# Optimization experiments

Hardware: AMD Instinct MI355X
Metric: run time of the kernel (lower is better)

The kernel has to match this reference:

```python
import jax, jax.numpy as jnp
import numpy as np

N_NODES = 100000
N_EDGES = 3200000
IN_DIM, HID_DIM, OUT_DIM = 384, 128, 5


def gcn_conv(x, src, dst, W, b, num_nodes):
    # PyG GCNConv: add self-loops, symmetric normalization, linear, aggregate, bias
    h = x @ W  # [N, out]
    ones = jnp.ones(src.shape[0], dtype=h.dtype)
    deg = jax.ops.segment_sum(ones, dst, num_segments=num_nodes)  # includes self-loops
    dinv = jnp.where(deg > 0, jax.lax.rsqrt(deg), 0.0)
    norm = dinv[src] * dinv[dst]  # [E+N]
    msg = h[src] * norm[:, None]
    out = jax.ops.segment_sum(msg, dst, num_segments=num_nodes)
    return out + b


def setup_inputs() -> dict:
    key = jax.random.key(0)
    ks = jax.random.split(key, 8)
    x = jax.random.normal(ks[0], (N_NODES, IN_DIM), dtype=jnp.float32)
    edge_index = jax.random.randint(ks[1], (2, N_EDGES), 0, N_NODES, dtype=jnp.int64)
    # Glorot-ish init for GCN linear weights
    def glorot(k, fi, fo):
        s = jnp.sqrt(6.0 / (fi + fo))
        return jax.random.uniform(k, (fi, fo), jnp.float32, -s, s)
    W1 = glorot(ks[2], IN_DIM, HID_DIM)
    b1 = jnp.zeros((HID_DIM,), jnp.float32)
    W2 = glorot(ks[3], HID_DIM, HID_DIM)
    b2 = jnp.zeros((HID_DIM,), jnp.float32)
    W3 = glorot(ks[4], HID_DIM, OUT_DIM)
    b3 = jnp.zeros((OUT_DIM,), jnp.float32)
    return {"x": x, "edge_index": edge_index, "W1": W1, "b1": b1,
            "W2": W2, "b2": b2, "W3": W3, "b3": b3}


def reference(x, edge_index, W1, b1, W2, b2, W3, b3):
    num_nodes = x.shape[0]
    loops = jnp.arange(num_nodes, dtype=edge_index.dtype)
    src = jnp.concatenate([edge_index[0], loops])
    dst = jnp.concatenate([edge_index[1], loops])
    # layer 1: GCNConv + ReLU (dropout is identity at inference)
    h = jax.nn.relu(gcn_conv(x, src, dst, W1, b1, num_nodes))
    # layer 2
    h = jax.nn.relu(gcn_conv(h, src, dst, W2, b2, num_nodes))
    # final layer: logits, no activation
    return gcn_conv(h, src, dst, W3, b3, num_nodes)
```

## Files before the change

kernel.cpp:

```cpp
#include <hip/hip_runtime.h>
#include <hip/hip_fp16.h>

#define NN 100000
#define NE 3200000
#define SCAN_CHUNK 1024

#define BSH 8
#define BKT_NODES 256
#define NBKT ((NN + BKT_NODES - 1) / BKT_NODES)
#define BIN_BLOCKS 256
#define EPB ((NE + BIN_BLOCKS - 1) / BIN_BLOCKS)
#define GH (NBKT * BIN_BLOCKS)

typedef unsigned int uint;
typedef unsigned short ushort;
typedef __attribute__((ext_vector_type(8))) _Float16 half8;
typedef __attribute__((ext_vector_type(4))) float f32x4;

__device__ inline void gload16(const void* g, void* l) {
    __builtin_amdgcn_global_load_lds(
        (const __attribute__((address_space(1))) void*)g,
        (__attribute__((address_space(3))) void*)l, 16, 0, 0);
}

__device__ inline uint f2h_pair(float a, float b) {
    return (uint)__half_as_ushort(__float2half(a)) |
           ((uint)__half_as_ushort(__float2half(b)) << 16);
}
__device__ inline float h2f_lo(uint u) { return __half2float(__ushort_as_half((ushort)(u & 0xFFFFu))); }
__device__ inline float h2f_hi(uint u) { return __half2float(__ushort_as_half((ushort)(u >> 16))); }
__device__ inline void splitH(float x, ushort& h, ushort& l) {
    __half hh = __float2half(x);
    h = __half_as_ushort(hh);
    l = __half_as_ushort(__float2half(x - __half2float(hh)));
}

__global__ __launch_bounds__(256) void hist_bkt(const int* __restrict__ dst,
                                                int* __restrict__ ghist) {
    __shared__ int h[NBKT];
    int t = threadIdx.x;
    for (int i = t; i < NBKT; i += 256) h[i] = 0;
    __syncthreads();
    int beg = blockIdx.x * EPB;
    int end = beg + EPB; if (end > NE) end = NE;
    for (int e = beg + t; e < end; e += 256)
        atomicAdd(&h[dst[e] >> BSH], 1);
    __syncthreads();
    for (int i = t; i < NBKT; i += 256)
        ghist[i * BIN_BLOCKS + blockIdx.x] = h[i];
}

__global__ __launch_bounds__(256) void scan_p1(const int* __restrict__ cnt,
                                               int* __restrict__ bsum, int N) {
    int t = threadIdx.x;
    int base = blockIdx.x * SCAN_CHUNK + t * 4;
    int s = 0;
#pragma unroll
    for (int q = 0; q < 4; q++) {
        int i = base + q;
        if (i < N) s += cnt[i];
    }
    __shared__ int red[4];
#pragma unroll
    for (int off = 32; off; off >>= 1) s += __shfl_down(s, off, 64);
    if ((t & 63) == 0) red[t >> 6] = s;
    __syncthreads();
    if (t == 0) bsum[blockIdx.x] = red[0] + red[1] + red[2] + red[3];
}

__global__ void scan_p2(int* __restrict__ bsum, int nb) {
    __shared__ int s[128];
    int t = threadIdx.x;
    int v = (t < nb) ? bsum[t] : 0;
    s[t] = v;
    __syncthreads();
    for (int off = 1; off < 128; off <<= 1) {
        int x = s[t];
        int add = (t >= off) ? s[t - off] : 0;
        __syncthreads();
        s[t] = x + add;
        __syncthreads();
    }
    if (t < nb) bsum[t] = s[t] - v;
}

__global__ __launch_bounds__(256) void scan_p3_plain(int* __restrict__ data,
                                                     const int* __restrict__ bsum, int N) {
    __shared__ int ts[256];
    int t = threadIdx.x;
    int base = blockIdx.x * SCAN_CHUNK + t * 4;
    int c[4];
    int s = 0;
#pragma unroll
    for (int q = 0; q < 4; q++) {
        int i = base + q;
        c[q] = (i < N) ? data[i] : 0;
        s += c[q];
    }
    ts[t] = s;
    __syncthreads();
    for (int off = 1; off < 256; off <<= 1) {
        int x = ts[t];
        int add = (t >= off) ? ts[t - off] : 0;
        __syncthreads();
        ts[t] = x + add;
        __syncthreads();
    }
    int run = bsum[blockIdx.x] + ts[t] - s;
#pragma unroll
    for (int q = 0; q < 4; q++) {
        int i = base + q;
        if (i < N) { data[i] = run; run += c[q]; }
    }
}

__global__ __launch_bounds__(256) void scan_p3_deg(const int* __restrict__ cnt,
                                                   const int* __restrict__ bsum,
                                                   int* __restrict__ rowptr,
                                                   float* __restrict__ dinv, int N) {
    __shared__ int ts[256];
    int t = threadIdx.x;
    int base = blockIdx.x * SCAN_CHUNK + t * 4;
    int c[4];
    int s = 0;
#pragma unroll
    for (int q = 0; q < 4; q++) {
        int i = base + q;
        c[q] = (i < N) ? cnt[i] : 0;
        s += c[q];
    }
    ts[t] = s;
    __syncthreads();
    for (int off = 1; off < 256; off <<= 1) {
        int x = ts[t];
        int add = (t >= off) ? ts[t - off] : 0;
        __syncthreads();
        ts[t] = x + add;
        __syncthreads();
    }
    int run = bsum[blockIdx.x] + ts[t] - s;
#pragma unroll
    for (int q = 0; q < 4; q++) {
        int i = base + q;
        if (i < N) {
            rowptr[i] = run;
            dinv[i] = 1.0f / sqrtf((float)(c[q] + 1));
            run += c[q];
        }
    }
    if (base < N && N <= base + 4) rowptr[N] = run;
}

__global__ __launch_bounds__(256) void bin_edges(const int* __restrict__ src,
                                                 const int* __restrict__ dst,
                                                 const int* __restrict__ ghist,
                                                 uint* __restrict__ binned) {
    __shared__ int cur[NBKT];
    int t = threadIdx.x;
    for (int i = t; i < NBKT; i += 256) cur[i] = ghist[i * BIN_BLOCKS + blockIdx.x];
    __syncthreads();
    int beg = blockIdx.x * EPB;
    int end = beg + EPB; if (end > NE) end = NE;
    for (int e = beg + t; e < end; e += 256) {
        int d = dst[e];
        int b = d >> BSH;
        int p = atomicAdd(&cur[b], 1);
        binned[p] = ((uint)src[e] << BSH) | (uint)(d & (BKT_NODES - 1));
    }
}

__global__ __launch_bounds__(256) void bucket_count(const uint* __restrict__ binned,
                                                    const int* __restrict__ ghist,
                                                    int* __restrict__ cnt) {
    __shared__ int c[BKT_NODES];
    int t = threadIdx.x;
    int bkt = blockIdx.x;
    for (int i = t; i < BKT_NODES; i += 256) c[i] = 0;
    __syncthreads();
    int beg = ghist[bkt * BIN_BLOCKS];
    int end = (bkt == NBKT - 1) ? NE : ghist[(bkt + 1) * BIN_BLOCKS];
    for (int j = beg + t; j < end; j += 256)
        atomicAdd(&c[binned[j] & (BKT_NODES - 1)], 1);
    __syncthreads();
    int base = bkt * BKT_NODES;
    int nb = NN - base; if (nb > BKT_NODES) nb = BKT_NODES;
    for (int i = t; i < nb; i += 256) cnt[base + i] = c[i];
}

__global__ __launch_bounds__(256) void csr_fill(const uint* __restrict__ binned,
                                                const int* __restrict__ ghist,
                                                const int* __restrict__ rowptr,
                                                int* __restrict__ col) {
    __shared__ int fill[BKT_NODES];
    int t = threadIdx.x;
    int bkt = blockIdx.x;
    for (int i = t; i < BKT_NODES; i += 256) fill[i] = 0;
    __syncthreads();
    int beg = ghist[bkt * BIN_BLOCKS];
    int end = (bkt == NBKT - 1) ? NE : ghist[(bkt + 1) * BIN_BLOCKS];
    int base = bkt * BKT_NODES;
    for (int j = beg + t; j < end; j += 256) {
        uint r = binned[j];
        int dl = r & (BKT_NODES - 1);
        int p = rowptr[base + dl] + atomicAdd(&fill[dl], 1);
        col[p] = (int)(r >> BSH);
    }
}

template <int K>
__global__ __launch_bounds__(256) void wsplit(const float* __restrict__ W,
                                              ushort* __restrict__ Wth,
                                              ushort* __restrict__ Wtl) {
    __shared__ float tile[32][128];
    int t = threadIdx.x;
    int kb = blockIdx.x;
    {
        int k = t >> 3, cq = t & 7;
#pragma unroll
        for (int q = 0; q < 4; q++) {
            float4 v = *(const float4*)&W[(size_t)(kb * 32 + k) * 128 + cq * 16 + q * 4];
            *(float4*)&tile[k][cq * 16 + q * 4] = v;
        }
    }
    __syncthreads();
    {
        int c = t >> 1, g = t & 1;
        ushort hs[16], ls[16];
#pragma unroll
        for (int i = 0; i < 16; i++) splitH(tile[g * 16 + i][c], hs[i], ls[i]);
        uint h[8], lo[8];
#pragma unroll
        for (int i = 0; i < 8; i++) {
            h[i] = (uint)hs[2 * i] | ((uint)hs[2 * i + 1] << 16);
            lo[i] = (uint)ls[2 * i] | ((uint)ls[2 * i + 1] << 16);
        }
        size_t o = (size_t)c * K + kb * 32 + g * 16;
        *(uint4*)&Wth[o] = make_uint4(h[0], h[1], h[2], h[3]);
        *(uint4*)&Wth[o + 8] = make_uint4(h[4], h[5], h[6], h[7]);
        *(uint4*)&Wtl[o] = make_uint4(lo[0], lo[1], lo[2], lo[3]);
        *(uint4*)&Wtl[o + 8] = make_uint4(lo[4], lo[5], lo[6], lo[7]);
    }
}

template <int K>
__global__ __launch_bounds__(256) void mfma_gemm_f32(const float* __restrict__ X,
                                                     const ushort* __restrict__ Wth,
                                                     const ushort* __restrict__ Wtl,
                                                     const float* __restrict__ dinv,
                                                     uint* __restrict__ Y, int M) {
    __shared__ char smem[24 * 1024];
    char* aP = smem;
    char* bH = smem + 8192;
    char* bL = smem + 16384;
    int tid = threadIdx.x;
    int w = tid >> 6, l = tid & 63;
    int rowBase = blockIdx.x * 128;

    f32x4 acc[2][8];
#pragma unroll
    for (int mf = 0; mf < 2; mf++)
#pragma unroll
        for (int n = 0; n < 8; n++) acc[mf][n] = (f32x4){0.f, 0.f, 0.f, 0.f};

    int sRow = tid >> 1, sKp = tid & 1;
    int gRow = rowBase + sRow;
    bool rowOK = gRow < M;
    size_t aBase = (size_t)(rowOK ? gRow : 0) * K + sKp * 16;

    float4 a0, a1, a2, a3;
    a0 = a1 = a2 = a3 = make_float4(0.f, 0.f, 0.f, 0.f);
    if (rowOK) {
        a0 = *(const float4*)&X[aBase];
        a1 = *(const float4*)&X[aBase + 4];
        a2 = *(const float4*)&X[aBase + 8];
        a3 = *(const float4*)&X[aBase + 12];
    }

    int fc = l & 15, fkg = l >> 4;
    int aoff0 = fkg * 2048 + ((2 * w + 0) * 16 + fc) * 16;
    int aoff1 = fkg * 2048 + ((2 * w + 1) * 16 + fc) * 16;

    for (int kt = 0; kt < K; kt += 32) {
#pragma unroll
        for (int i = 0; i < 2; i++) {
            int cb = (i * 4 + w) * 64;
            int c = cb + l;
            int kg = c >> 7, colb = c & 127;
            size_t go = (size_t)colb * K + kt + kg * 8;
            gload16(&Wth[go], bH + cb * 16);
            gload16(&Wtl[go], bL + cb * 16);
        }
        {
            float v[16] = {a0.x, a0.y, a0.z, a0.w, a1.x, a1.y, a1.z, a1.w,
                           a2.x, a2.y, a2.z, a2.w, a3.x, a3.y, a3.z, a3.w};
            uint hh[8];
#pragma unroll
            for (int i = 0; i < 8; i++) hh[i] = f2h_pair(v[2 * i], v[2 * i + 1]);
            *(uint4*)(aP + (2 * sKp) * 2048 + sRow * 16) = make_uint4(hh[0], hh[1], hh[2], hh[3]);
            *(uint4*)(aP + (2 * sKp + 1) * 2048 + sRow * 16) = make_uint4(hh[4], hh[5], hh[6], hh[7]);
        }
        __syncthreads();

        if (kt + 32 < K && rowOK) {
            size_t nb = aBase + kt + 32;
            a0 = *(const float4*)&X[nb];
            a1 = *(const float4*)&X[nb + 4];
            a2 = *(const float4*)&X[nb + 8];
            a3 = *(const float4*)&X[nb + 12];
        }

        half8 av0 = *(const half8*)(aP + aoff0);
        half8 av1 = *(const half8*)(aP + aoff1);
#pragma unroll
        for (int n = 0; n < 8; n++) {
            int boff = fkg * 2048 + (16 * n + fc) * 16;
            half8 bh = *(const half8*)(bH + boff);
            half8 bl = *(const half8*)(bL + boff);
            acc[0][n] = __builtin_amdgcn_mfma_f32_16x16x32_f16(av0, bh, acc[0][n], 0, 0, 0);
            acc[0][n] = __builtin_amdgcn_mfma_f32_16x16x32_f16(av0, bl, acc[0][n], 0, 0, 0);
            acc[1][n] = __builtin_amdgcn_mfma_f32_16x16x32_f16(av1, bh, acc[1][n], 0, 0, 0);
            acc[1][n] = __builtin_amdgcn_mfma_f32_16x16x32_f16(av1, bl, acc[1][n], 0, 0, 0);
        }
        __syncthreads();
    }

#pragma unroll
    for (int mf = 0; mf < 2; mf++) {
        float dscale[4];
#pragma unroll
        for (int r = 0; r < 4; r++) {
            int row = rowBase + (2 * w + mf) * 16 + fkg * 4 + r;
            dscale[r] = (row < M) ? dinv[row] : 0.f;
        }
#pragma unroll
        for (int n = 0; n < 8; n++) {
#pragma unroll
            for (int r = 0; r < 4; r++) {
                float val = acc[mf][n][r] * dscale[r];
                float p = __shfl_xor(val, 1, 64);
                int row = rowBase + (2 * w + mf) * 16 + fkg * 4 + r;
                if (!(l & 1) && row < M)
                    Y[(size_t)row * 64 + 8 * n + (fc >> 1)] = f2h_pair(val, p);
            }
        }
    }
}

__global__ __launch_bounds__(256) void mfma_gemm_f16(const ushort* __restrict__ Xh,
                                                     const ushort* __restrict__ Wth,
                                                     const ushort* __restrict__ Wtl,
                                                     const float* __restrict__ dinv,
                                                     uint* __restrict__ Y, int M) {
    __shared__ char smem[24 * 1024];
    char* aP = smem;
    char* bH = smem + 8192;
    char* bL = smem + 16384;
    int tid = threadIdx.x;
    int w = tid >> 6, l = tid & 63;
    int rowBase = blockIdx.x * 128;

    f32x4 acc[2][8];
#pragma unroll
    for (int mf = 0; mf < 2; mf++)
#pragma unroll
        for (int n = 0; n < 8; n++) acc[mf][n] = (f32x4){0.f, 0.f, 0.f, 0.f};

    int fc = l & 15, fkg = l >> 4;
    int aoff0 = fkg * 2048 + ((2 * w + 0) * 16 + fc) * 16;
    int aoff1 = fkg * 2048 + ((2 * w + 1) * 16 + fc) * 16;

    for (int kt = 0; kt < 128; kt += 32) {
#pragma unroll
        for (int i = 0; i < 2; i++) {
            int cb = (i * 4 + w) * 64;
            int c = cb + l;
            int kg = c >> 7, idx = c & 127;
            gload16(&Xh[(size_t)(rowBase + idx) * 128 + kt + kg * 8], aP + cb * 16);
            gload16(&Wth[(size_t)idx * 128 + kt + kg * 8], bH + cb * 16);
            gload16(&Wtl[(size_t)idx * 128 + kt + kg * 8], bL + cb * 16);
        }
        __syncthreads();
        half8 av0 = *(const half8*)(aP + aoff0);
        half8 av1 = *(const half8*)(aP + aoff1);
#pragma unroll
        for (int n = 0; n < 8; n++) {
            int boff = fkg * 2048 + (16 * n + fc) * 16;
            half8 bh = *(const half8*)(bH + boff);
            half8 bl = *(const half8*)(bL + boff);
            acc[0][n] = __builtin_amdgcn_mfma_f32_16x16x32_f16(av0, bh, acc[0][n], 0, 0, 0);
            acc[0][n] = __builtin_amdgcn_mfma_f32_16x16x32_f16(av0, bl, acc[0][n], 0, 0, 0);
            acc[1][n] = __builtin_amdgcn_mfma_f32_16x16x32_f16(av1, bh, acc[1][n], 0, 0, 0);
            acc[1][n] = __builtin_amdgcn_mfma_f32_16x16x32_f16(av1, bl, acc[1][n], 0, 0, 0);
        }
        __syncthreads();
    }

#pragma unroll
    for (int mf = 0; mf < 2; mf++) {
        float dscale[4];
#pragma unroll
        for (int r = 0; r < 4; r++) {
            int row = rowBase + (2 * w + mf) * 16 + fkg * 4 + r;
            dscale[r] = (row < M) ? dinv[row] : 0.f;
        }
#pragma unroll
        for (int n = 0; n < 8; n++) {
#pragma unroll
            for (int r = 0; r < 4; r++) {
                float val = acc[mf][n][r] * dscale[r];
                float p = __shfl_xor(val, 1, 64);
                int row = rowBase + (2 * w + mf) * 16 + fkg * 4 + r;
                if (!(l & 1) && row < M)
                    Y[(size_t)row * 64 + 8 * n + (fc >> 1)] = f2h_pair(val, p);
            }
        }
    }
}

__global__ __launch_bounds__(256) void gemm_n5h(const uint4* __restrict__ Xh,
                                                const float* __restrict__ W,
                                                float* __restrict__ Y, int M) {
    __shared__ float wl[640];
    int t = threadIdx.x;
    for (int i = t; i < 640; i += 256) wl[i] = W[i];
    __syncthreads();
    int row = blockIdx.x * 256 + t;
    if (row >= M) return;
    float acc0 = 0.f, acc1 = 0.f, acc2 = 0.f, acc3 = 0.f, acc4 = 0.f;
#pragma unroll
    for (int kq = 0; kq < 16; kq++) {
        uint4 v = Xh[(size_t)row * 16 + kq];
        uint uu[4] = {v.x, v.y, v.z, v.w};
#pragma unroll
        for (int e = 0; e < 4; e++) {
            float x0 = h2f_lo(uu[e]);
            float x1 = h2f_hi(uu[e]);
            int k = kq * 8 + e * 2;
            acc0 = fmaf(x0, wl[k * 5 + 0], acc0); acc0 = fmaf(x1, wl[k * 5 + 5], acc0);
            acc1 = fmaf(x0, wl[k * 5 + 1], acc1); acc1 = fmaf(x1, wl[k * 5 + 6], acc1);
            acc2 = fmaf(x0, wl[k * 5 + 2], acc2); acc2 = fmaf(x1, wl[k * 5 + 7], acc2);
            acc3 = fmaf(x0, wl[k * 5 + 3], acc3); acc3 = fmaf(x1, wl[k * 5 + 8], acc3);
            acc4 = fmaf(x0, wl[k * 5 + 4], acc4); acc4 = fmaf(x1, wl[k * 5 + 9], acc4);
        }
    }
    Y[row * 5 + 0] = acc0;
    Y[row * 5 + 1] = acc1;
    Y[row * 5 + 2] = acc2;
    Y[row * 5 + 3] = acc3;
    Y[row * 5 + 4] = acc4;
}

__global__ void pack5(const float* __restrict__ Y, const float* __restrict__ dinv,
                      uint4* __restrict__ hc, int N) {
    int node = blockIdx.x * 256 + threadIdx.x;
    if (node >= N) return;
    float di = dinv[node];
    float v0 = Y[node * 5 + 0] * di;
    float v1 = Y[node * 5 + 1] * di;
    float v2 = Y[node * 5 + 2] * di;
    float v3 = Y[node * 5 + 3] * di;
    float v4 = Y[node * 5 + 4] * di;
    hc[node] = make_uint4(f2h_pair(v0, v1), f2h_pair(v2, v3), f2h_pair(v4, 0.f), 0u);
}

#define ACC8H(v)                              \
    a0 += h2f_lo(v.x); a1 += h2f_hi(v.x);     \
    a2 += h2f_lo(v.y); a3 += h2f_hi(v.y);     \
    a4 += h2f_lo(v.z); a5 += h2f_hi(v.z);     \
    a6 += h2f_lo(v.w); a7 += h2f_hi(v.w);

__global__ __launch_bounds__(256) void agg128_v3(const uint4* __restrict__ hb4,
                                                 const int* __restrict__ rowptr,
                                                 const int* __restrict__ col,
                                                 const float* __restrict__ dinv,
                                                 const float* __restrict__ bias,
                                                 uint4* __restrict__ out, int N, int do_relu) {
    int wave = threadIdx.x >> 6;
    int lane = threadIdx.x & 63;
    int node = blockIdx.x * 4 + wave;
    if (node >= N) return;
    int g = lane >> 4;
    int q = lane & 15;
    int beg = rowptr[node], end = rowptr[node + 1];
    float a0 = 0.f, a1 = 0.f, a2 = 0.f, a3 = 0.f, a4 = 0.f, a5 = 0.f, a6 = 0.f, a7 = 0.f;

    int j = beg;
    for (; j + 16 <= end; j += 16) {
        int s0 = col[j + g];
        int s1 = col[j + 4 + g];
        int s2 = col[j + 8 + g];
        int s3 = col[j + 12 + g];
        uint4 v0 = hb4[(size_t)s0 * 16 + q];
        uint4 v1 = hb4[(size_t)s1 * 16 + q];
        uint4 v2 = hb4[(size_t)s2 * 16 + q];
        uint4 v3 = hb4[(size_t)s3 * 16 + q];
        ACC8H(v0); ACC8H(v1); ACC8H(v2); ACC8H(v3);
    }
    if (j + 8 <= end) {
        int s0 = col[j + g];
        int s1 = col[j + 4 + g];
        uint4 v0 = hb4[(size_t)s0 * 16 + q];
        uint4 v1 = hb4[(size_t)s1 * 16 + q];
        ACC8H(v0); ACC8H(v1);
        j += 8;
    }
    if (j < end) {
        int jj0 = j + g, jj1 = j + 4 + g;
        bool p0 = jj0 < end, p1 = jj1 < end;
        int s0 = p0 ? col[jj0] : node;
        int s1 = p1 ? col[jj1] : node;
        uint4 v0 = hb4[(size_t)s0 * 16 + q];
        uint4 v1 = hb4[(size_t)s1 * 16 + q];
        if (!p0) v0 = make_uint4(0u, 0u, 0u, 0u);
        if (!p1) v1 = make_uint4(0u, 0u, 0u, 0u);
        ACC8H(v0); ACC8H(v1);
    }
#pragma unroll
    for (int off = 16; off <= 32; off <<= 1) {
        a0 += __shfl_xor(a0, off, 64);
        a1 += __shfl_xor(a1, off, 64);
        a2 += __shfl_xor(a2, off, 64);
        a3 += __shfl_xor(a3, off, 64);
        a4 += __shfl_xor(a4, off, 64);
        a5 += __shfl_xor(a5, off, 64);
        a6 += __shfl_xor(a6, off, 64);
        a7 += __shfl_xor(a7, off, 64);
    }
    if (g == 0) {
        uint4 vs = hb4[(size_t)node * 16 + q];
        ACC8H(vs);
        float di = dinv[node];
        const float4* bias4 = (const float4*)bias;
        float4 bb0 = bias4[q * 2], bb1 = bias4[q * 2 + 1];
        float o0 = a0 * di + bb0.x, o1 = a1 * di + bb0.y;
        float o2 = a2 * di + bb0.z, o3 = a3 * di + bb0.w;
        float o4 = a4 * di + bb1.x, o5 = a5 * di + bb1.y;
        float o6 = a6 * di + bb1.z, o7 = a7 * di + bb1.w;
        if (do_relu) {
            o0 = fmaxf(o0, 0.f); o1 = fmaxf(o1, 0.f);
            o2 = fmaxf(o2, 0.f); o3 = fmaxf(o3, 0.f);
            o4 = fmaxf(o4, 0.f); o5 = fmaxf(o5, 0.f);
            o6 = fmaxf(o6, 0.f); o7 = fmaxf(o7, 0.f);
        }
        out[(size_t)node * 16 + q] =
            make_uint4(f2h_pair(o0, o1), f2h_pair(o2, o3), f2h_pair(o4, o5), f2h_pair(o6, o7));
    }
}

__global__ void agg5_v2(const uint4* __restrict__ hc, const int* __restrict__ rowptr,
                        const int* __restrict__ col, const float* __restrict__ dinv,
                        const float* __restrict__ b3, float* __restrict__ out, int N) {
    int node = blockIdx.x * 256 + threadIdx.x;
    if (node >= N) return;
    float a0 = 0.f, a1 = 0.f, a2 = 0.f, a3 = 0.f, a4 = 0.f;
    int beg = rowptr[node], end = rowptr[node + 1];
#pragma unroll 2
    for (int j = beg; j < end; ++j) {
        uint4 v = hc[col[j]];
        a0 += h2f_lo(v.x); a1 += h2f_hi(v.x);
        a2 += h2f_lo(v.y); a3 += h2f_hi(v.y);
        a4 += h2f_lo(v.z);
    }
    uint4 vs = hc[node];
    a0 += h2f_lo(vs.x); a1 += h2f_hi(vs.x);
    a2 += h2f_lo(vs.y); a3 += h2f_hi(vs.y);
    a4 += h2f_lo(vs.z);
    float di = dinv[node];
    out[node * 5 + 0] = a0 * di + b3[0];
    out[node * 5 + 1] = a1 * di + b3[1];
    out[node * 5 + 2] = a2 * di + b3[2];
    out[node * 5 + 3] = a3 * di + b3[3];
    out[node * 5 + 4] = a4 * di + b3[4];
}

static inline size_t align512(size_t x) { return (x + 511) & ~(size_t)511; }

extern "C" void kernel_launch(void* const* d_in, const int* in_sizes, int n_in,
                              void* d_out, int out_size, void* d_ws, size_t ws_size,
                              hipStream_t stream) {
    const float* x  = (const float*)d_in[0];
    const int* ei   = (const int*)d_in[1];
    const float* W1 = (const float*)d_in[2];
    const float* b1 = (const float*)d_in[3];
    const float* W2 = (const float*)d_in[4];
    const float* b2 = (const float*)d_in[5];
    const float* W3 = (const float*)d_in[6];
    const float* b3 = (const float*)d_in[7];
    const int* src = ei;
    const int* dst = ei + NE;

    char* ws = (char*)d_ws;
    size_t off = 0;
    int* cnt = (int*)(ws + off);        off += align512((size_t)NN * 4);
    int* rowptr = (int*)(ws + off);     off += align512((size_t)(NN + 1) * 4);
    float* dinv = (float*)(ws + off);   off += align512((size_t)NN * 4);
    int* bsum = (int*)(ws + off);       off += align512((size_t)128 * 4);
    int* ghist = (int*)(ws + off);      off += align512((size_t)GH * 4);
    ushort* wt1h = (ushort*)(ws + off); off += align512((size_t)128 * 384 * 2);
    ushort* wt1l = (ushort*)(ws + off); off += align512((size_t)128 * 384 * 2);
    ushort* wt2h = (ushort*)(ws + off); off += align512((size_t)128 * 128 * 2);
    ushort* wt2l = (ushort*)(ws + off); off += align512((size_t)128 * 128 * 2);
    int* col = (int*)(ws + off);        off += align512((size_t)NE * 4);
    uint* hb = (uint*)(ws + off);       off += align512((size_t)NN * 64 * 4);
    char* bufF = (char*)(ws + off);     off += align512((size_t)NN * 128 * 4);
    float* bufC = (float*)(ws + off);   off += align512((size_t)NN * 5 * 4);
    uint4* hc = (uint4*)(ws + off);     off += align512((size_t)NN * 16);
    uint* binned = (uint*)bufF;
    (void)ws_size;

    wsplit<384><<<12, 256, 0, stream>>>(W1, wt1h, wt1l);
    wsplit<128><<<4, 256, 0, stream>>>(W2, wt2h, wt2l);

    hist_bkt<<<BIN_BLOCKS, 256, 0, stream>>>(dst, ghist);
    {
        int nb = (GH + SCAN_CHUNK - 1) / SCAN_CHUNK;
        scan_p1<<<nb, 256, 0, stream>>>(ghist, bsum, GH);
        scan_p2<<<1, 128, 0, stream>>>(bsum, nb);
        scan_p3_plain<<<nb, 256, 0, stream>>>(ghist, bsum, GH);
    }
    bin_edges<<<BIN_BLOCKS, 256, 0, stream>>>(src, dst, ghist, binned);
    bucket_count<<<NBKT, 256, 0, stream>>>(binned, ghist, cnt);
    {
        int nb = (NN + SCAN_CHUNK - 1) / SCAN_CHUNK;
        scan_p1<<<nb, 256, 0, stream>>>(cnt, bsum, NN);
        scan_p2<<<1, 128, 0, stream>>>(bsum, nb);
        scan_p3_deg<<<nb, 256, 0, stream>>>(cnt, bsum, rowptr, dinv, NN);
    }
    csr_fill<<<NBKT, 256, 0, stream>>>(binned, ghist, rowptr, col);

    int gemm_blocks = (NN + 127) / 128;
    mfma_gemm_f32<384><<<gemm_blocks, 256, 0, stream>>>(x, wt1h, wt1l, dinv, hb, NN);
    agg128_v3<<<(NN + 3) / 4, 256, 0, stream>>>((const uint4*)hb, rowptr, col, dinv, b1,
                                                (uint4*)bufF, NN, 1);
    mfma_gemm_f16<<<gemm_blocks, 256, 0, stream>>>((const ushort*)bufF, wt2h, wt2l, dinv, hb, NN);
    agg128_v3<<<(NN + 3) / 4, 256, 0, stream>>>((const uint4*)hb, rowptr, col, dinv, b2,
                                                (uint4*)bufF, NN, 1);
    gemm_n5h<<<(NN + 255) / 256, 256, 0, stream>>>((const uint4*)bufF, W3, bufC, NN);
    pack5<<<(NN + 255) / 256, 256, 0, stream>>>(bufC, dinv, hc, NN);
    agg5_v2<<<(NN + 255) / 256, 256, 0, stream>>>(hc, rowptr, col, dinv, b3, (float*)d_out, NN);
}
```

Measured before the change: 427.8 us.

## Fuse bucket scan into rowptr, stream fp32 A via LDS DMA, fuse pack5

Three changes. First, the per-bucket count is combined with a local block scan, so rowptr and dinv come out of one kernel and the three-kernel node scan is removed. This works because buckets are contiguous in binned order, so the bucket's start offset equals the global offset. Second, the first-layer GEMM now loads fp32 X tiles directly into LDS with global_load_lds and converts them to fp16 at fragment-read time, replacing register prefetch plus an fp16 LDS store. This drops the software prefetch overlap and doubles the A tile's LDS footprint. Third, the final n=5 GEMM writes dinv-scaled packed halves directly, which eliminates the pack5 kernel and its intermediate buffer.

```diff
diff --git a/kernel.cpp b/kernel.cpp
--- a/kernel.cpp
+++ b/kernel.cpp
@@ -112,43 +112,6 @@
         int i = base + q;
         if (i < N) { data[i] = run; run += c[q]; }
     }
-}
-
-__global__ __launch_bounds__(256) void scan_p3_deg(const int* __restrict__ cnt,
-                                                   const int* __restrict__ bsum,
-                                                   int* __restrict__ rowptr,
-                                                   float* __restrict__ dinv, int N) {
-    __shared__ int ts[256];
-    int t = threadIdx.x;
-    int base = blockIdx.x * SCAN_CHUNK + t * 4;
-    int c[4];
-    int s = 0;
-#pragma unroll
-    for (int q = 0; q < 4; q++) {
-        int i = base + q;
-        c[q] = (i < N) ? cnt[i] : 0;
-        s += c[q];
-    }
-    ts[t] = s;
-    __syncthreads();
-    for (int off = 1; off < 256; off <<= 1) {
-        int x = ts[t];
-        int add = (t >= off) ? ts[t - off] : 0;
-        __syncthreads();
-        ts[t] = x + add;
-        __syncthreads();
-    }
-    int run = bsum[blockIdx.x] + ts[t] - s;
-#pragma unroll
-    for (int q = 0; q < 4; q++) {
-        int i = base + q;
-        if (i < N) {
-            rowptr[i] = run;
-            dinv[i] = 1.0f / sqrtf((float)(c[q] + 1));
-            run += c[q];
-        }
-    }
-    if (base < N && N <= base + 4) rowptr[N] = run;
 }
 
 __global__ __launch_bounds__(256) void bin_edges(const int* __restrict__ src,
@@ -169,22 +132,37 @@
     }
 }
 
-__global__ __launch_bounds__(256) void bucket_count(const uint* __restrict__ binned,
-                                                    const int* __restrict__ ghist,
-                                                    int* __restrict__ cnt) {
+__global__ __launch_bounds__(256) void bucket_rowptr(const uint* __restrict__ binned,
+                                                     const int* __restrict__ ghist,
+                                                     int* __restrict__ rowptr,
+                                                     float* __restrict__ dinv) {
     __shared__ int c[BKT_NODES];
+    __shared__ int ts[256];
     int t = threadIdx.x;
     int bkt = blockIdx.x;
-    for (int i = t; i < BKT_NODES; i += 256) c[i] = 0;
+    c[t] = 0;
     __syncthreads();
     int beg = ghist[bkt * BIN_BLOCKS];
     int end = (bkt == NBKT - 1) ? NE : ghist[(bkt + 1) * BIN_BLOCKS];
     for (int j = beg + t; j < end; j += 256)
         atomicAdd(&c[binned[j] & (BKT_NODES - 1)], 1);
     __syncthreads();
-    int base = bkt * BKT_NODES;
-    int nb = NN - base; if (nb > BKT_NODES) nb = BKT_NODES;
-    for (int i = t; i < nb; i += 256) cnt[base + i] = c[i];
+    int ci = c[t];
+    ts[t] = ci;
+    __syncthreads();
+    for (int off = 1; off < 256; off <<= 1) {
+        int x = ts[t];
+        int add = (t >= off) ? ts[t - off] : 0;
+        __syncthreads();
+        ts[t] = x + add;
+        __syncthreads();
+    }
+    int node = bkt * BKT_NODES + t;
+    if (node < NN) {
+        rowptr[node] = beg + ts[t] - ci;
+        dinv[node] = 1.0f / sqrtf((float)(ci + 1));
+    }
+    if (bkt == 0 && t == 0) rowptr[NN] = NE;
 }
 
 __global__ __launch_bounds__(256) void csr_fill(const uint* __restrict__ binned,
@@ -248,10 +226,10 @@
                                                      const ushort* __restrict__ Wtl,
                                                      const float* __restrict__ dinv,
                                                      uint* __restrict__ Y, int M) {
-    __shared__ char smem[24 * 1024];
-    char* aP = smem;
-    char* bH = smem + 8192;
-    char* bL = smem + 16384;
+    __shared__ char smem[32 * 1024];
+    char* aF = smem;
+    char* bH = smem + 16384;
+    char* bL = smem + 24576;
     int tid = threadIdx.x;
     int w = tid >> 6, l = tid & 63;
     int rowBase = blockIdx.x * 128;
@@ -262,25 +240,18 @@
 #pragma unroll
         for (int n = 0; n < 8; n++) acc[mf][n] = (f32x4){0.f, 0.f, 0.f, 0.f};
 
-    int sRow = tid >> 1, sKp = tid & 1;
-    int gRow = rowBase + sRow;
-    bool rowOK = gRow < M;
-    size_t aBase = (size_t)(rowOK ? gRow : 0) * K + sKp * 16;
-
-    float4 a0, a1, a2, a3;
-    a0 = a1 = a2 = a3 = make_float4(0.f, 0.f, 0.f, 0.f);
-    if (rowOK) {
-        a0 = *(const float4*)&X[aBase];
-        a1 = *(const float4*)&X[aBase + 4];
-        a2 = *(const float4*)&X[aBase + 8];
-        a3 = *(const float4*)&X[aBase + 12];
-    }
-
     int fc = l & 15, fkg = l >> 4;
-    int aoff0 = fkg * 2048 + ((2 * w + 0) * 16 + fc) * 16;
-    int aoff1 = fkg * 2048 + ((2 * w + 1) * 16 + fc) * 16;
 
     for (int kt = 0; kt < K; kt += 32) {
+#pragma unroll
+        for (int i = 0; i < 4; i++) {
+            int cb = (i * 4 + w) * 64;
+            int c = cb + l;
+            int kq = c >> 7, row = c & 127;
+            int gr = rowBase + row;
+            if (gr >= M) gr = 0;
+            gload16(&X[(size_t)gr * K + kt + kq * 4], aF + cb * 16);
+        }
 #pragma unroll
         for (int i = 0; i < 2; i++) {
             int cb = (i * 4 + w) * 64;
@@ -290,36 +261,26 @@
             gload16(&Wth[go], bH + cb * 16);
             gload16(&Wtl[go], bL + cb * 16);
         }
-        {
-            float v[16] = {a0.x, a0.y, a0.z, a0.w, a1.x, a1.y, a1.z, a1.w,
-                           a2.x, a2.y, a2.z, a2.w, a3.x, a3.y, a3.z, a3.w};
-            uint hh[8];
-#pragma unroll
-            for (int i = 0; i < 8; i++) hh[i] = f2h_pair(v[2 * i], v[2 * i + 1]);
-            *(uint4*)(aP + (2 * sKp) * 2048 + sRow * 16) = make_uint4(hh[0], hh[1], hh[2], hh[3]);
-            *(uint4*)(aP + (2 * sKp + 1) * 2048 + sRow * 16) = make_uint4(hh[4], hh[5], hh[6], hh[7]);
-        }
-        __syncthreads();
-
-        if (kt + 32 < K && rowOK) {
-            size_t nb = aBase + kt + 32;
-            a0 = *(const float4*)&X[nb];
-            a1 = *(const float4*)&X[nb + 4];
-            a2 = *(const float4*)&X[nb + 8];
-            a3 = *(const float4*)&X[nb + 12];
-        }
-
-        half8 av0 = *(const half8*)(aP + aoff0);
-        half8 av1 = *(const half8*)(aP + aoff1);
-#pragma unroll
-        for (int n = 0; n < 8; n++) {
-            int boff = fkg * 2048 + (16 * n + fc) * 16;
-            half8 bh = *(const half8*)(bH + boff);
-            half8 bl = *(const half8*)(bL + boff);
-            acc[0][n] = __builtin_amdgcn_mfma_f32_16x16x32_f16(av0, bh, acc[0][n], 0, 0, 0);
-            acc[0][n] = __builtin_amdgcn_mfma_f32_16x16x32_f16(av0, bl, acc[0][n], 0, 0, 0);
-            acc[1][n] = __builtin_amdgcn_mfma_f32_16x16x32_f16(av1, bh, acc[1][n], 0, 0, 0);
-            acc[1][n] = __builtin_amdgcn_mfma_f32_16x16x32_f16(av1, bl, acc[1][n], 0, 0, 0);
+        __syncthreads();
+
+#pragma unroll
+        for (int mf = 0; mf < 2; mf++) {
+            int mrow = (2 * w + mf) * 16 + fc;
+            f32x4 p0 = *(const f32x4*)(aF + (2 * fkg) * 2048 + mrow * 16);
+            f32x4 p1 = *(const f32x4*)(aF + (2 * fkg + 1) * 2048 + mrow * 16);
+            half8 av;
+            av[0] = (_Float16)p0[0]; av[1] = (_Float16)p0[1];
+            av[2] = (_Float16)p0[2]; av[3] = (_Float16)p0[3];
+            av[4] = (_Float16)p1[0]; av[5] = (_Float16)p1[1];
+            av[6] = (_Float16)p1[2]; av[7] = (_Float16)p1[3];
+#pragma unroll
+            for (int n = 0; n < 8; n++) {
+                int boff = fkg * 2048 + (16 * n + fc) * 16;
+                half8 bh = *(const half8*)(bH + boff);
+                half8 bl = *(const half8*)(bL + boff);
+                acc[mf][n] = __builtin_amdgcn_mfma_f32_16x16x32_f16(av, bh, acc[mf][n], 0, 0, 0);
+                acc[mf][n] = __builtin_amdgcn_mfma_f32_16x16x32_f16(av, bl, acc[mf][n], 0, 0, 0);
+            }
         }
         __syncthreads();
     }
@@ -419,7 +380,8 @@
 
 __global__ __launch_bounds__(256) void gemm_n5h(const uint4* __restrict__ Xh,
                                                 const float* __restrict__ W,
-                                                float* __restrict__ Y, int M) {
+                                                const float* __restrict__ dinv,
+                                                uint4* __restrict__ hc, int M) {
     __shared__ float wl[640];
     int t = threadIdx.x;
     for (int i = t; i < 640; i += 256) wl[i] = W[i];
@@ -443,24 +405,10 @@
             acc4 = fmaf(x0, wl[k * 5 + 4], acc4); acc4 = fmaf(x1, wl[k * 5 + 9], acc4);
         }
     }
-    Y[row * 5 + 0] = acc0;
-    Y[row * 5 + 1] = acc1;
-    Y[row * 5 + 2] = acc2;
-    Y[row * 5 + 3] = acc3;
-    Y[row * 5 + 4] = acc4;
-}
-
-__global__ void pack5(const float* __restrict__ Y, const float* __restrict__ dinv,
-                      uint4* __restrict__ hc, int N) {
-    int node = blockIdx.x * 256 + threadIdx.x;
-    if (node >= N) return;
-    float di = dinv[node];
-    float v0 = Y[node * 5 + 0] * di;
-    float v1 = Y[node * 5 + 1] * di;
-    float v2 = Y[node * 5 + 2] * di;
-    float v3 = Y[node * 5 + 3] * di;
-    float v4 = Y[node * 5 + 4] * di;
-    hc[node] = make_uint4(f2h_pair(v0, v1), f2h_pair(v2, v3), f2h_pair(v4, 0.f), 0u);
+    float di = dinv[row];
+    hc[row] = make_uint4(f2h_pair(acc0 * di, acc1 * di),
+                         f2h_pair(acc2 * di, acc3 * di),
+                         f2h_pair(acc4 * di, 0.f), 0u);
 }
 
 #define ACC8H(v)                              \
@@ -591,7 +539,6 @@
 
     char* ws = (char*)d_ws;
     size_t off = 0;
-    int* cnt = (int*)(ws + off);        off += align512((size_t)NN * 4);
     int* rowptr = (int*)(ws + off);     off += align512((size_t)(NN + 1) * 4);
     float* dinv = (float*)(ws + off);   off += align512((size_t)NN * 4);
     int* bsum = (int*)(ws + off);       off += align512((size_t)128 * 4);
@@ -603,7 +550,6 @@
     int* col = (int*)(ws + off);        off += align512((size_t)NE * 4);
     uint* hb = (uint*)(ws + off);       off += align512((size_t)NN * 64 * 4);
     char* bufF = (char*)(ws + off);     off += align512((size_t)NN * 128 * 4);
-    float* bufC = (float*)(ws + off);   off += align512((size_t)NN * 5 * 4);
     uint4* hc = (uint4*)(ws + off);     off += align512((size_t)NN * 16);
     uint* binned = (uint*)bufF;
     (void)ws_size;
@@ -619,13 +565,7 @@
         scan_p3_plain<<<nb, 256, 0, stream>>>(ghist, bsum, GH);
     }
     bin_edges<<<BIN_BLOCKS, 256, 0, stream>>>(src, dst, ghist, binned);
-    bucket_count<<<NBKT, 256, 0, stream>>>(binned, ghist, cnt);
-    {
-        int nb = (NN + SCAN_CHUNK - 1) / SCAN_CHUNK;
-        scan_p1<<<nb, 256, 0, stream>>>(cnt, bsum, NN);
-        scan_p2<<<1, 128, 0, stream>>>(bsum, nb);
-        scan_p3_deg<<<nb, 256, 0, stream>>>(cnt, bsum, rowptr, dinv, NN);
-    }
+    bucket_rowptr<<<NBKT, 256, 0, stream>>>(binned, ghist, rowptr, dinv);
     csr_fill<<<NBKT, 256, 0, stream>>>(binned, ghist, rowptr, col);
 
     int gemm_blocks = (NN + 127) / 128;
@@ -635,7 +575,6 @@
     mfma_gemm_f16<<<gemm_blocks, 256, 0, stream>>>((const ushort*)bufF, wt2h, wt2l, dinv, hb, NN);
     agg128_v3<<<(NN + 3) / 4, 256, 0, stream>>>((const uint4*)hb, rowptr, col, dinv, b2,
                                                 (uint4*)bufF, NN, 1);
-    gemm_n5h<<<(NN + 255) / 256, 256, 0, stream>>>((const uint4*)bufF, W3, bufC, NN);
-    pack5<<<(NN + 255) / 256, 256, 0, stream>>>(bufC, dinv, hc, NN);
+    gemm_n5h<<<(NN + 255) / 256, 256, 0, stream>>>((const uint4*)bufF, W3, dinv, hc, NN);
     agg5_v2<<<(NN + 255) / 256, 256, 0, stream>>>(hc, rowptr, col, dinv, b3, (float*)d_out, NN);
 }
```

Result: slower. 461.2 us (+7.8%).
